# Performance work log

Measured on AMD Instinct MI355X. Metric: run time of the kernel, lower is better.

The kernel has to match this reference:

```python
import jax, jax.numpy as jnp
import numpy as np

T, N, C, L, H, NA, NL = 32, 64, 64, 64, 256, 16, 128


def _gru_dir(x, wi, wh, bi, bh):
    # x: [Lt, N, H] time-major; PyTorch GRU gate order (r, z, n). Returns [Lt, N, H].
    xi = jnp.einsum('tnh,gh->tng', x, wi) + bi  # precompute input projections [Lt,N,3H]
    def step(h, gi):
        gh = h @ wh.T + bh
        ir, iz, inn = jnp.split(gi, 3, -1)
        hr, hz, hn = jnp.split(gh, 3, -1)
        r = jax.nn.sigmoid(ir + hr)
        z = jax.nn.sigmoid(iz + hz)
        n = jnp.tanh(inn + r * hn)
        hnew = (1.0 - z) * n + z * h
        return hnew, hnew
    h0 = jnp.zeros((x.shape[1], wh.shape[1]), x.dtype)
    _, ys = jax.lax.scan(step, h0, xi)
    return ys


def setup_inputs() -> dict:
    key = jax.random.key(0)
    ks = jax.random.split(key, 32)
    s = 0.05
    p = {}
    p['condition'] = jax.random.normal(ks[0], (T, N, C), jnp.float32)
    p['lines'] = jax.random.randint(ks[1], (N, L), 0, NL)
    p['a_idx'] = jax.random.randint(ks[2], (T, N), 0, NA)
    p['p_idx'] = jax.random.randint(ks[3], (T, N), 0, L)
    p['embed'] = jax.random.normal(ks[4], (NL, H)) * s
    p['aemb'] = jax.random.normal(ks[5], (NA, H)) * s
    p['gru_wi_f'] = jax.random.normal(ks[6], (3 * H, H)) * s
    p['gru_wh_f'] = jax.random.normal(ks[7], (3 * H, H)) * s
    p['gru_bi_f'] = jax.random.normal(ks[8], (3 * H,)) * s
    p['gru_bh_f'] = jax.random.normal(ks[9], (3 * H,)) * s
    p['gru_wi_b'] = jax.random.normal(ks[10], (3 * H, H)) * s
    p['gru_wh_b'] = jax.random.normal(ks[11], (3 * H, H)) * s
    p['gru_bi_b'] = jax.random.normal(ks[12], (3 * H,)) * s
    p['gru_bh_b'] = jax.random.normal(ks[13], (3 * H,)) * s
    p['f_w1'] = jax.random.normal(ks[14], (H, C + H)) * s
    p['f_b1'] = jax.random.normal(ks[15], (H,)) * s
    p['f_w2'] = jax.random.normal(ks[16], (H, H)) * s
    p['f_b2'] = jax.random.normal(ks[17], (H,)) * s
    p['cell_wi'] = jax.random.normal(ks[18], (3 * H, H)) * s
    p['cell_wh'] = jax.random.normal(ks[19], (3 * H, H)) * s
    p['cell_bi'] = jax.random.normal(ks[20], (3 * H,)) * s
    p['cell_bh'] = jax.random.normal(ks[21], (3 * H,)) * s
    p['critic_w'] = jax.random.normal(ks[22], (1, H)) * s
    p['critic_b'] = jax.random.normal(ks[23], (1,)) * s
    p['pointer_w'] = jax.random.normal(ks[24], (L, H)) * s
    p['pointer_b'] = jax.random.normal(ks[25], (L,)) * s
    p['actor_w'] = jax.random.normal(ks[26], (NA, H)) * s
    p['actor_b'] = jax.random.normal(ks[27], (NA,)) * s
    p['query_w'] = jax.random.normal(ks[28], (H, H)) * s
    p['query_b'] = jax.random.normal(ks[29], (H,)) * s
    return p


def reference(condition, lines, a_idx, p_idx, embed, aemb,
              gru_wi_f, gru_wh_f, gru_bi_f, gru_bh_f,
              gru_wi_b, gru_wh_b, gru_bi_b, gru_bh_b,
              f_w1, f_b1, f_w2, f_b2,
              cell_wi, cell_wh, cell_bi, cell_bh,
              critic_w, critic_b, pointer_w, pointer_b,
              actor_w, actor_b, query_w, query_b):
    Tn, Nn = a_idx.shape
    Ln = lines.shape[1]
    Hd = embed.shape[1]
    M = embed[lines]                           # [N,L,H]
    x = jnp.transpose(M, (1, 0, 2))            # [L,N,H] time-major
    # torch.roll(x, shifts=i): rolled[i, j] = x[(j - i) % L]
    idx = (jnp.arange(Ln)[None, :] - jnp.arange(Ln)[:, None]) % Ln
    rolled = x[idx]                            # [L_roll, L_time, N, H]
    def bigru(seq):
        f = _gru_dir(seq, gru_wi_f, gru_wh_f, gru_bi_f, gru_bh_f)
        b = _gru_dir(seq[::-1], gru_wi_b, gru_wh_b, gru_bi_b, gru_bh_b)[::-1]
        return jnp.concatenate([f, b], -1)     # [L_time,N,2H]
    K1 = jax.vmap(bigru)(rolled)               # [L,L,N,2H]
    K = K1.reshape(Ln, Ln, Nn, 2, Hd).transpose(2, 0, 1, 3, 4).reshape(Nn, Ln, 2 * Ln, Hd)
    # A[t-1] for t=0 is hx.a == 0 (fresh episode, zero hidden state)
    a_prev = jnp.concatenate([jnp.zeros((1, Nn), a_idx.dtype), a_idx[:-1]], 0)
    rng_n = jnp.arange(Nn)
    def step(h, inp):
        cond_t, ap_t, p_t, a_t = inp
        obs = jnp.concatenate([cond_t, aemb[ap_t]], -1)
        xf = jax.nn.relu(obs @ f_w1.T + f_b1)
        xf = jax.nn.relu(xf @ f_w2.T + f_b2)
        gi = xf @ cell_wi.T + cell_bi
        gh = h @ cell_wh.T + cell_bh
        ir, iz, inn = jnp.split(gi, 3, -1)
        hr, hz, hn = jnp.split(gh, 3, -1)
        r = jax.nn.sigmoid(ir + hr)
        z = jax.nn.sigmoid(iz + hz)
        n = jnp.tanh(inn + r * hn)
        h = (1.0 - z) * n + z * h
        p_probs = jax.nn.softmax(h @ pointer_w.T + pointer_b, -1)
        q = h @ query_w.T + query_b
        k = K[rng_n, p_t]                      # gather: [N, 2L, H]
        l = jnp.einsum('nkh,nh->nk', k, q)
        zz = jnp.einsum('nk,nkh->nh', l, k)
        a_probs = jax.nn.softmax(zz @ actor_w.T + actor_b, -1)
        v = h @ critic_w.T + critic_b
        out = jnp.concatenate([a_t[:, None].astype(h.dtype), p_t[:, None].astype(h.dtype),
                               v, h, a_probs, p_probs], -1)
        return h, out
    h0 = jnp.zeros((Nn, Hd), condition.dtype)
    _, hxs = jax.lax.scan(step, h0, (condition, a_prev, p_idx, a_idx))
    return hxs  # packed RecurrentState: [T, N, 1+1+1+H+na+L]
```

## Files before the change

### kernel.cpp

```cpp
#include <hip/hip_runtime.h>
#include <hip/hip_bf16.h>
#include <cstddef>
#include <cstdint>

typedef __bf16 bf16;
typedef bf16 bf16x8 __attribute__((ext_vector_type(8)));
typedef float f32x4 __attribute__((ext_vector_type(4)));

#define DEV static __device__ __forceinline__

DEV f32x4 mfma_bf16(bf16x8 a, bf16x8 b, f32x4 c) {
  return __builtin_amdgcn_mfma_f32_16x16x32_bf16(a, b, c, 0, 0, 0);
}
DEV f32x4 mfma_fp8(long a, long b, f32x4 c) {
  return __builtin_amdgcn_mfma_f32_16x16x32_fp8_fp8(a, b, c, 0, 0, 0);
}

DEV float sigmoid_f(float x) {
  return __builtin_amdgcn_rcpf(1.0f + __expf(-x));
}
DEV float tanh_f(float x) {
  float ax = fabsf(x);
  float e = __expf(-2.0f * ax);
  float t = 1.0f - 2.0f * e * __builtin_amdgcn_rcpf(1.0f + e);
  return copysignf(t, x);
}
DEV unsigned char fp8_of(float x) {
  return (unsigned char)(__builtin_amdgcn_cvt_pk_fp8_f32(x, x, 0, false) & 0xFF);
}

static constexpr int H_ = 256;

static constexpr int o_embed = 0;
static constexpr int o_aemb = 32768;
static constexpr int o_wi_f = 36864;
static constexpr int o_wh_f = 233472;
static constexpr int o_bi_f = 430080;
static constexpr int o_bh_f = 430848;
static constexpr int o_wi_b = 431616;
static constexpr int o_wh_b = 628224;
static constexpr int o_bi_b = 824832;
static constexpr int o_bh_b = 825600;
static constexpr int o_f_w1 = 826368;
static constexpr int o_f_b1 = 908288;
static constexpr int o_f_w2 = 908544;
static constexpr int o_f_b2 = 974080;
static constexpr int o_cell_wi = 974336;
static constexpr int o_cell_wh = 1170944;
static constexpr int o_cell_bi = 1367552;
static constexpr int o_cell_bh = 1368320;
static constexpr int o_critic_w = 1369088;
static constexpr int o_critic_b = 1369344;
static constexpr int o_pointer_w = 1369360;
static constexpr int o_pointer_b = 1385744;
static constexpr int o_actor_w = 1385808;
static constexpr int o_actor_b = 1389904;
static constexpr int o_query_w = 1389920;
static constexpr int o_query_b = 1455456;
static constexpr int CW_TOTAL = 1455712;
static constexpr int WH8_TOTAL = 393216;
static constexpr int PREP_TOTAL = CW_TOTAL + WH8_TOTAL;
static constexpr int PREP_WGS = (PREP_TOTAL + 2047) / 2048;

static constexpr size_t XI_OFF = 0;
static constexpr size_t XI_BYTES = 2ull * 4096 * 768 * 2;
static constexpr size_t K1_OFF = XI_OFF + XI_BYTES;
static constexpr size_t K1_BYTES = 64ull * 32 * 128 * 256;
static constexpr size_t GI_OFF = K1_OFF + K1_BYTES;
static constexpr size_t GI_BYTES = 32ull * 64 * 768 * 4;
static constexpr size_t HD_OFF = GI_OFF + GI_BYTES;
static constexpr size_t HD_BYTES = 32ull * 64 * 256 * 4;
static constexpr size_t SLOT_OFF = HD_OFF + HD_BYTES;
static constexpr size_t SLOT_BYTES = 64ull * 64 * 4;
static constexpr size_t FLG_OFF = SLOT_OFF + SLOT_BYTES;
static constexpr size_t FLG_BYTES = 256;
static constexpr size_t WL_OFF = FLG_OFF + FLG_BYTES;
static constexpr size_t WL_BYTES = 8448;
static constexpr size_t CW_OFF = WL_OFF + WL_BYTES;
static constexpr size_t CW_BYTES = (size_t)CW_TOTAL * 2;
static constexpr size_t WH8_OFF = ((CW_OFF + CW_BYTES + 255) / 256) * 256;

struct PrepArgs {
  const void* src[26];
  int off[26];
  int cnt[26];
};

__global__ __launch_bounds__(256)
void k_prep(PrepArgs pa, const uint32_t* __restrict__ cond, const uint32_t* __restrict__ emb,
            const void* __restrict__ whf_src, const void* __restrict__ whb_src,
            const int* __restrict__ p_idx, int* __restrict__ flags,
            bf16* __restrict__ cw, unsigned char* __restrict__ wh8,
            int* __restrict__ slot_map, int* __restrict__ wl) {
  int bx = blockIdx.x;
  int tid = threadIdx.x;
  __shared__ int votes[256];

  int c1 = 0;
  {
    uint32_t w0 = emb[tid * 2], w1 = emb[tid * 2 + 1];
    int e0 = (int)((w0 >> 7) & 0xFF), e1 = (int)((w1 >> 7) & 0xFF);
    c1 += (e0 >= 96 && e0 <= 130) ? 1 : 0;
    c1 += (e1 >= 96 && e1 <= 130) ? 1 : 0;
  }
  votes[tid] = c1;
  __syncthreads();
  __shared__ int f32w_s;
  if (tid == 0) {
    int s = 0;
    for (int i = 0; i < 256; i++) s += votes[i];
    f32w_s = (s < 256) ? 1 : 0;
  }
  __syncthreads();
  bool f32w = f32w_s != 0;

  if (bx == 0) {
    __syncthreads();
    int c0 = 0;
    {
      uint32_t w0 = cond[tid * 2], w1 = cond[tid * 2 + 1];
      int e0 = (int)((w0 >> 7) & 0xFF), e1 = (int)((w1 >> 7) & 0xFF);
      c0 += (e0 >= 96 && e0 <= 130) ? 1 : 0;
      c0 += (e1 >= 96 && e1 <= 130) ? 1 : 0;
    }
    votes[tid] = c0;
    __syncthreads();
    if (tid == 0) {
      int s = 0;
      for (int i = 0; i < 256; i++) s += votes[i];
      flags[0] = (s < 256) ? 1 : 0;
      flags[1] = f32w ? 1 : 0;
    }
  }

  if (bx < PREP_WGS) {
    int gidx = bx * 2048 + tid;
    for (int e = 0; e < 8; e++, gidx += 256) {
      if (gidx >= PREP_TOTAL) break;
      if (gidx < CW_TOTAL) {
        int rem = gidx, s = 0;
        while (s < 26 && rem >= pa.cnt[s]) { rem -= pa.cnt[s]; s++; }
        if (s < 26) {
          float v = f32w ? ((const float*)pa.src[s])[rem]
                         : (float)((const bf16*)pa.src[s])[rem];
          cw[pa.off[s] + rem] = (bf16)v;
        }
      } else {
        int i = gidx - CW_TOTAL;
        const void* src = (i < 196608) ? whf_src : whb_src;
        int k = (i < 196608) ? i : i - 196608;
        float v = f32w ? ((const float*)src)[k] : (float)((const bf16*)src)[k];
        wh8[i] = fp8_of(v);
      }
    }
    return;
  }

  __shared__ int pbuf[2048];
  __shared__ signed char sm[4096];
  __shared__ unsigned short entL[8 * 512];
  __shared__ int cntL[8];
  for (int i = tid; i < 2048; i += 256) pbuf[i] = p_idx[i];
  for (int i = tid; i < 4096; i += 256) sm[i] = -1;
  __syncthreads();
  if (tid < 64) {
    int n = tid, cnt = 0;
    for (int t = 0; t < 32; t++) {
      int p = pbuf[t * 64 + n];
      if (sm[n * 64 + p] < 0) sm[n * 64 + p] = (signed char)(cnt++);
    }
  }
  __syncthreads();
  for (int i = tid; i < 4096; i += 256) slot_map[i] = (int)sm[i];
  if (tid < 8) {
    int xcd = tid, cnt = 0;
    for (int roll = xcd * 8; roll < xcd * 8 + 8; roll++)
      for (int n = 0; n < 64; n++)
        if (sm[n * 64 + roll] >= 0) entL[xcd * 512 + (cnt++)] = (unsigned short)(n | (roll << 8));
    unsigned short pad = (unsigned short)((xcd * 8) << 8);
    while (cnt & 15) entL[xcd * 512 + (cnt++)] = pad;
    cntL[xcd] = cnt;
  }
  __syncthreads();
  if (tid < 8) wl[tid] = cntL[tid] >> 4;
  unsigned short* we = (unsigned short*)((char*)wl + 64);
  for (int i = tid; i < 8 * 512; i += 256) we[i] = entL[i];
}

__global__ __launch_bounds__(256)
void k_xi_gi(const int* __restrict__ lines, const bf16* __restrict__ cw,
             const void* __restrict__ cond_raw, const int* __restrict__ flags,
             const int* __restrict__ a_idx, bf16* __restrict__ xi,
             float* __restrict__ gi) {
  int bx = blockIdx.x;
  int tid = threadIdx.x;
  int w = tid >> 6, l = tid & 63, quad = l >> 4, l15 = l & 15;
  __shared__ __attribute__((aligned(16))) bf16 s_a[32 * 328];
  __shared__ __attribute__((aligned(16))) bf16 s_b[32 * 264];

  if (bx < 256) {
    int dir = bx & 1, rb = bx >> 1;
    const bf16* embed = cw + o_embed;
    const bf16* wi = cw + (dir ? o_wi_b : o_wi_f);
    const bf16* bi = cw + (dir ? o_bi_b : o_bi_f);
    bf16* xs = s_a;
    {
      int row = tid >> 3, seg = tid & 7;
      int grow = rb * 32 + row;
      int u = grow >> 6, n = grow & 63;
      int line = lines[n * 64 + u];
      const bf16* src = embed + (size_t)line * H_ + seg * 32;
      bf16* dst = xs + row * 264 + seg * 32;
#pragma unroll
      for (int e = 0; e < 4; e++) *(bf16x8*)(dst + e * 8) = *(const bf16x8*)(src + e * 8);
    }
    __syncthreads();
    f32x4 acc[2][12];
#pragma unroll
    for (int mt = 0; mt < 2; mt++)
#pragma unroll
      for (int nt = 0; nt < 12; nt++) acc[mt][nt] = f32x4{0.f, 0.f, 0.f, 0.f};
#pragma unroll
    for (int ks = 0; ks < 8; ks++) {
      int koff = ks * 32 + quad * 8;
      bf16x8 a0 = *(const bf16x8*)(xs + l15 * 264 + koff);
      bf16x8 a1 = *(const bf16x8*)(xs + (l15 + 16) * 264 + koff);
#pragma unroll
      for (int nt = 0; nt < 12; nt++) {
        int g = (w * 12 + nt) * 16 + l15;
        bf16x8 b = *(const bf16x8*)(wi + (size_t)g * H_ + koff);
        acc[0][nt] = mfma_bf16(a0, b, acc[0][nt]);
        acc[1][nt] = mfma_bf16(a1, b, acc[1][nt]);
      }
    }
    size_t base = (size_t)dir * 4096 * 768;
#pragma unroll
    for (int nt = 0; nt < 12; nt++) {
      int g = (w * 12 + nt) * 16 + l15;
      float bias = (float)bi[g];
#pragma unroll
      for (int mt = 0; mt < 2; mt++)
#pragma unroll
        for (int r = 0; r < 4; r++) {
          int m = mt * 16 + quad * 4 + r;
          xi[base + (size_t)(rb * 32 + m) * 768 + g] = (bf16)(acc[mt][nt][r] + bias);
        }
    }
    return;
  }

  int rb = bx - 256;
  const bf16* aemb = cw + o_aemb;
  const bf16* f_w1 = cw + o_f_w1;
  const bf16* f_b1 = cw + o_f_b1;
  const bf16* f_w2 = cw + o_f_w2;
  const bf16* f_b2 = cw + o_f_b2;
  const bf16* cell_wi = cw + o_cell_wi;
  const bf16* cell_bi = cw + o_cell_bi;
  bool cf32 = flags[0] != 0;
  bf16* obs = s_a;
  bf16* xf1 = s_b;

  for (int e = tid; e < 32 * 320; e += 256) {
    int row = e / 320, col = e - row * 320;
    int grow = rb * 32 + row;
    int t = grow >> 6, n = grow & 63;
    float v;
    if (col < 64) {
      v = cf32 ? ((const float*)cond_raw)[(size_t)grow * 64 + col]
               : (float)((const bf16*)cond_raw)[(size_t)grow * 64 + col];
    } else {
      int ap = (t == 0) ? 0 : a_idx[(t - 1) * 64 + n];
      v = (float)aemb[ap * 256 + (col - 64)];
    }
    obs[row * 328 + col] = (bf16)v;
  }
  __syncthreads();
  {
    f32x4 acc[2][4];
#pragma unroll
    for (int mt = 0; mt < 2; mt++)
#pragma unroll
      for (int nt = 0; nt < 4; nt++) acc[mt][nt] = f32x4{0.f, 0.f, 0.f, 0.f};
#pragma unroll
    for (int ks = 0; ks < 10; ks++) {
      int koff = ks * 32 + quad * 8;
      bf16x8 a0 = *(const bf16x8*)(obs + l15 * 328 + koff);
      bf16x8 a1 = *(const bf16x8*)(obs + (l15 + 16) * 328 + koff);
#pragma unroll
      for (int nt = 0; nt < 4; nt++) {
        int g = (w * 4 + nt) * 16 + l15;
        bf16x8 b = *(const bf16x8*)(f_w1 + (size_t)g * 320 + koff);
        acc[0][nt] = mfma_bf16(a0, b, acc[0][nt]);
        acc[1][nt] = mfma_bf16(a1, b, acc[1][nt]);
      }
    }
#pragma unroll
    for (int nt = 0; nt < 4; nt++) {
      int g = (w * 4 + nt) * 16 + l15;
      float bias = (float)f_b1[g];
#pragma unroll
      for (int mt = 0; mt < 2; mt++)
#pragma unroll
        for (int r = 0; r < 4; r++) {
          int m = mt * 16 + quad * 4 + r;
          xf1[m * 264 + g] = (bf16)fmaxf(acc[mt][nt][r] + bias, 0.f);
        }
    }
  }
  __syncthreads();
  bf16* xf2 = obs;
  {
    f32x4 acc[2][4];
#pragma unroll
    for (int mt = 0; mt < 2; mt++)
#pragma unroll
      for (int nt = 0; nt < 4; nt++) acc[mt][nt] = f32x4{0.f, 0.f, 0.f, 0.f};
#pragma unroll
    for (int ks = 0; ks < 8; ks++) {
      int koff = ks * 32 + quad * 8;
      bf16x8 a0 = *(const bf16x8*)(xf1 + l15 * 264 + koff);
      bf16x8 a1 = *(const bf16x8*)(xf1 + (l15 + 16) * 264 + koff);
#pragma unroll
      for (int nt = 0; nt < 4; nt++) {
        int g = (w * 4 + nt) * 16 + l15;
        bf16x8 b = *(const bf16x8*)(f_w2 + (size_t)g * 256 + koff);
        acc[0][nt] = mfma_bf16(a0, b, acc[0][nt]);
        acc[1][nt] = mfma_bf16(a1, b, acc[1][nt]);
      }
    }
#pragma unroll
    for (int nt = 0; nt < 4; nt++) {
      int g = (w * 4 + nt) * 16 + l15;
      float bias = (float)f_b2[g];
#pragma unroll
      for (int mt = 0; mt < 2; mt++)
#pragma unroll
        for (int r = 0; r < 4; r++) {
          int m = mt * 16 + quad * 4 + r;
          xf2[m * 264 + g] = (bf16)fmaxf(acc[mt][nt][r] + bias, 0.f);
        }
    }
  }
  __syncthreads();
  {
    f32x4 acc[2][12];
#pragma unroll
    for (int mt = 0; mt < 2; mt++)
#pragma unroll
      for (int nt = 0; nt < 12; nt++) acc[mt][nt] = f32x4{0.f, 0.f, 0.f, 0.f};
#pragma unroll
    for (int ks = 0; ks < 8; ks++) {
      int koff = ks * 32 + quad * 8;
      bf16x8 a0 = *(const bf16x8*)(xf2 + l15 * 264 + koff);
      bf16x8 a1 = *(const bf16x8*)(xf2 + (l15 + 16) * 264 + koff);
#pragma unroll
      for (int nt = 0; nt < 12; nt++) {
        int g = (w * 12 + nt) * 16 + l15;
        bf16x8 b = *(const bf16x8*)(cell_wi + (size_t)g * 256 + koff);
        acc[0][nt] = mfma_bf16(a0, b, acc[0][nt]);
        acc[1][nt] = mfma_bf16(a1, b, acc[1][nt]);
      }
    }
#pragma unroll
    for (int nt = 0; nt < 12; nt++) {
      int g = (w * 12 + nt) * 16 + l15;
      float bias = (float)cell_bi[g];
#pragma unroll
      for (int mt = 0; mt < 2; mt++)
#pragma unroll
        for (int r = 0; r < 4; r++) {
          int m = mt * 16 + quad * 4 + r;
          gi[(size_t)(rb * 32 + m) * 768 + g] = acc[mt][nt][r] + bias;
        }
    }
  }
}

__global__ __launch_bounds__(1024)
void k_main(const bf16* __restrict__ cw, const unsigned char* __restrict__ wh8,
            const bf16* __restrict__ xi, const int* __restrict__ slot_map,
            const int* __restrict__ wl, const float* __restrict__ gi,
            unsigned char* __restrict__ K1c, float* __restrict__ hdec) {
  int bx = blockIdx.x;
  int tid = threadIdx.x;
  int w = tid >> 6, l = tid & 63, quad = l >> 4, l15 = l & 15;
  int c = w * 16 + l15;
  __shared__ __attribute__((aligned(16))) unsigned char smem[2][16 * 264 * 2];

  if (bx < 512) {
    int xcd = bx & 7, dir = (bx >> 3) & 1, slot = bx >> 4;
    if (slot >= wl[xcd]) return;
    const unsigned short* we = (const unsigned short*)((const char*)wl + 64) + xcd * 512 + slot * 16;
    const unsigned char* whd = wh8 + (size_t)dir * 196608;
    const bf16* bh = cw + (dir ? o_bh_b : o_bh_f);

    unsigned char (*hb)[16 * 264 * 2] = smem;
    for (int idx = tid; idx < 16 * 264; idx += 1024) hb[0][idx] = 0;

    int rollv[4], nbase[4];
#pragma unroll
    for (int r = 0; r < 4; r++) {
      int e = we[quad * 4 + r];
      rollv[r] = e >> 8;
      nbase[r] = (e & 255) * 768;
    }
    int crow = tid >> 6, cseg = tid & 63;
    int ec = we[crow];
    int n_c = ec & 255, roll_c = ec >> 8;
    int kslot = slot_map[n_c * 64 + roll_c];
    unsigned char* dstb = K1c + ((size_t)n_c * 32 + (kslot < 0 ? 0 : kslot)) * 32768 + cseg * 4;

    float hreg[4] = {0.f, 0.f, 0.f, 0.f};
    float bhv[3];
    const unsigned char* bp[3];
#pragma unroll
    for (int g = 0; g < 3; g++) {
      int grow = g * 256 + c;
      bhv[g] = (float)bh[grow];
      bp[g] = whd + (size_t)grow * 256 + quad * 8;
    }
    const bf16* xid = xi + (size_t)dir * 4096 * 768;
    __syncthreads();

    bf16 xpre[3][4];
#pragma unroll
    for (int r = 0; r < 4; r++) {
      int u = dir ? ((63 - rollv[r]) & 63) : ((0 - rollv[r]) & 63);
      const bf16* xr = xid + u * 49152 + nbase[r] + c;
#pragma unroll
      for (int g = 0; g < 3; g++) xpre[g][r] = xr[g * 256];
    }

    int cur = 0;
    for (int t = 0; t < 64; t++) {
      int j = dir ? (63 - t) : t;
      bf16 xnx[3][4];
#pragma unroll
      for (int r = 0; r < 4; r++) {
        int u = dir ? ((62 - t - rollv[r]) & 63) : ((t + 1 - rollv[r]) & 63);
        const bf16* xr = xid + u * 49152 + nbase[r] + c;
#pragma unroll
        for (int g = 0; g < 3; g++) xnx[g][r] = xr[g * 256];
      }

      f32x4 acc[3];
#pragma unroll
      for (int g = 0; g < 3; g++) acc[g] = f32x4{0.f, 0.f, 0.f, 0.f};
#pragma unroll
      for (int ks = 0; ks < 8; ks++) {
        int ko = ks * 32 + quad * 8;
        long a0 = *(const long*)(hb[cur] + l15 * 264 + ko);
#pragma unroll
        for (int g = 0; g < 3; g++) {
          long b = *(const long*)(bp[g] + ks * 32);
          acc[g] = mfma_fp8(a0, b, acc[g]);
        }
      }
      int nxt = cur ^ 1;
#pragma unroll
      for (int r = 0; r < 4; r++) {
        float rg = sigmoid_f((float)xpre[0][r] + acc[0][r] + bhv[0]);
        float zg = sigmoid_f((float)xpre[1][r] + acc[1][r] + bhv[1]);
        float ng = tanh_f((float)xpre[2][r] + rg * (acc[2][r] + bhv[2]));
        hreg[r] = (1.f - zg) * ng + zg * hreg[r];
        hb[nxt][(quad * 4 + r) * 264 + c] = fp8_of(hreg[r]);
      }
      __syncthreads();
      if (kslot >= 0) {
        *(uint32_t*)(dstb + (size_t)(j * 2 + dir) * 256) =
            *(const uint32_t*)(hb[nxt] + crow * 264 + cseg * 4);
      }
#pragma unroll
      for (int g = 0; g < 3; g++)
#pragma unroll
        for (int r = 0; r < 4; r++) xpre[g][r] = xnx[g][r];
      cur = nxt;
    }
    return;
  }

  int nq = bx - 512;
  const bf16* wh = cw + o_cell_wh;
  const bf16* bh = cw + o_cell_bh;
  bf16 (*hb)[16 * 264] = (bf16(*)[16 * 264])smem;
  for (int idx = tid; idx < 16 * 264; idx += 1024) hb[0][idx] = (bf16)0.f;

  float hreg[4] = {0.f, 0.f, 0.f, 0.f};
  float bhv[3];
  const bf16* bp[3];
  int goff[3][4];
#pragma unroll
  for (int g = 0; g < 3; g++) {
    int grow = g * 256 + c;
    bhv[g] = (float)bh[grow];
    bp[g] = wh + (size_t)grow * 256 + quad * 8;
#pragma unroll
    for (int r = 0; r < 4; r++)
      goff[g][r] = (quad * 4 + r) * 768 + grow;
  }
  const float* gbase = gi + (size_t)nq * 16 * 768;
  __syncthreads();

  float gpre[3][4];
#pragma unroll
  for (int r = 0; r < 4; r++)
#pragma unroll
    for (int g = 0; g < 3; g++) gpre[g][r] = gbase[goff[g][r]];

  int cur = 0;
  for (int t = 0; t < 32; t++) {
    int tp = (t + 1) & 31;
    const float* gr = gbase + (size_t)tp * 64 * 768;
    float gnx[3][4];
#pragma unroll
    for (int r = 0; r < 4; r++)
#pragma unroll
      for (int g = 0; g < 3; g++) gnx[g][r] = gr[goff[g][r]];

    f32x4 acc[3];
#pragma unroll
    for (int g = 0; g < 3; g++) acc[g] = f32x4{0.f, 0.f, 0.f, 0.f};
#pragma unroll
    for (int ks = 0; ks < 8; ks++) {
      int ko = ks * 32 + quad * 8;
      bf16x8 a0 = *(const bf16x8*)(hb[cur] + l15 * 264 + ko);
#pragma unroll
      for (int g = 0; g < 3; g++) {
        bf16x8 b = *(const bf16x8*)(bp[g] + ks * 32);
        acc[g] = mfma_bf16(a0, b, acc[g]);
      }
    }
    int nxt = cur ^ 1;
#pragma unroll
    for (int r = 0; r < 4; r++) {
      float rg = sigmoid_f(gpre[0][r] + acc[0][r] + bhv[0]);
      float zg = sigmoid_f(gpre[1][r] + acc[1][r] + bhv[1]);
      float ng = tanh_f(gpre[2][r] + rg * (acc[2][r] + bhv[2]));
      float hnew = (1.f - zg) * ng + zg * hreg[r];
      hreg[r] = hnew;
      hb[nxt][(quad * 4 + r) * 264 + c] = (bf16)hnew;
      hdec[((size_t)t * 64 + nq * 16 + quad * 4 + r) * 256 + c] = hnew;
    }
    __syncthreads();
#pragma unroll
    for (int g = 0; g < 3; g++)
#pragma unroll
      for (int r = 0; r < 4; r++) gpre[g][r] = gnx[g][r];
    cur = nxt;
  }
}

__global__ __launch_bounds__(256)
void k_post(const float* __restrict__ hdec, const unsigned char* __restrict__ K1c,
            const int* __restrict__ slot_map, const int* __restrict__ flags,
            const int* __restrict__ a_idx, const int* __restrict__ p_idx,
            const bf16* __restrict__ cw, void* __restrict__ out_raw) {
  int bx = blockIdx.x;
  int tid = threadIdx.x;
  int w = tid >> 6, l = tid & 63, quad = l >> 4, l15 = l & 15;
  __shared__ __attribute__((aligned(16))) unsigned char sraw[38032];
  bool f32o = flags[1] != 0;

  if (bx < 64) {
    int rb = bx;
    const bf16* pointer_w = cw + o_pointer_w;
    const bf16* pointer_b = cw + o_pointer_b;
    const bf16* critic_w = cw + o_critic_w;
    const bf16* critic_b = cw + o_critic_b;
    bf16* hsb = (bf16*)sraw;
    float* pls = (float*)(sraw + 16896);
    float* vred = (float*)(sraw + 16896 + 8448);

    for (int idx = tid; idx < 32 * 256; idx += 256) {
      int row = idx >> 8, col = idx & 255;
      hsb[row * 264 + col] = (bf16)hdec[(size_t)(rb * 32 + row) * 256 + col];
    }
    __syncthreads();

    {
      f32x4 acc[2];
      acc[0] = f32x4{0.f, 0.f, 0.f, 0.f};
      acc[1] = f32x4{0.f, 0.f, 0.f, 0.f};
      int g = w * 16 + l15;
#pragma unroll
      for (int ks = 0; ks < 8; ks++) {
        int koff = ks * 32 + quad * 8;
        bf16x8 a0 = *(const bf16x8*)(hsb + l15 * 264 + koff);
        bf16x8 a1 = *(const bf16x8*)(hsb + (l15 + 16) * 264 + koff);
        bf16x8 b = *(const bf16x8*)(pointer_w + (size_t)g * 256 + koff);
        acc[0] = mfma_bf16(a0, b, acc[0]);
        acc[1] = mfma_bf16(a1, b, acc[1]);
      }
      float bias = (float)pointer_b[g];
#pragma unroll
      for (int mt = 0; mt < 2; mt++)
#pragma unroll
        for (int r = 0; r < 4; r++) {
          int m = mt * 16 + quad * 4 + r;
          pls[m * 66 + g] = acc[mt][r] + bias;
        }
    }
    {
      int row = tid >> 3, seg = tid & 7;
      float acc = 0.f;
#pragma unroll
      for (int k = 0; k < 32; k++)
        acc += (float)hsb[row * 264 + seg * 32 + k] * (float)critic_w[seg * 32 + k];
      vred[row * 8 + seg] = acc;
    }
    __syncthreads();

    if (tid < 32) {
      float mx = -1e30f;
      for (int k = 0; k < 64; k++) mx = fmaxf(mx, pls[tid * 66 + k]);
      float sm = 0.f;
      for (int k = 0; k < 64; k++) {
        float e = __expf(pls[tid * 66 + k] - mx);
        pls[tid * 66 + k] = e;
        sm += e;
      }
      float inv = __builtin_amdgcn_rcpf(sm);
      for (int k = 0; k < 64; k++) pls[tid * 66 + k] *= inv;
      float v = (float)critic_b[0];
      for (int s = 0; s < 8; s++) v += vred[tid * 8 + s];
      vred[tid * 8] = v;
    }
    __syncthreads();

    if (f32o) {
      float* ob = (float*)out_raw;
      if (tid < 32) {
        int grow = rb * 32 + tid;
        ob[(size_t)grow * 339 + 0] = (float)a_idx[grow];
        ob[(size_t)grow * 339 + 1] = (float)p_idx[grow];
        ob[(size_t)grow * 339 + 2] = vred[tid * 8];
      }
      for (int idx = tid; idx < 32 * 256; idx += 256) {
        int row = idx >> 8, col = idx & 255;
        int grow = rb * 32 + row;
        ob[(size_t)grow * 339 + 3 + col] = hdec[(size_t)grow * 256 + col];
      }
      for (int idx = tid; idx < 32 * 64; idx += 256) {
        int row = idx >> 6, col = idx & 63;
        ob[(size_t)(rb * 32 + row) * 339 + 275 + col] = pls[row * 66 + col];
      }
    } else {
      bf16* ob = (bf16*)out_raw;
      if (tid < 32) {
        int grow = rb * 32 + tid;
        ob[(size_t)grow * 339 + 0] = (bf16)(float)a_idx[grow];
        ob[(size_t)grow * 339 + 1] = (bf16)(float)p_idx[grow];
        ob[(size_t)grow * 339 + 2] = (bf16)vred[tid * 8];
      }
      for (int idx = tid; idx < 32 * 256; idx += 256) {
        int row = idx >> 8, col = idx & 255;
        int grow = rb * 32 + row;
        ob[(size_t)grow * 339 + 3 + col] = (bf16)hdec[(size_t)grow * 256 + col];
      }
      for (int idx = tid; idx < 32 * 64; idx += 256) {
        int row = idx >> 6, col = idx & 63;
        ob[(size_t)(rb * 32 + row) * 339 + 275 + col] = (bf16)pls[row * 66 + col];
      }
    }
    return;
  }

  int tn = bx - 64;
  int t = tn >> 6, n = tn & 63;
  const bf16* actor_w = cw + o_actor_w;
  const bf16* actor_b = cw + o_actor_b;
  const bf16* query_w = cw + o_query_w;
  const bf16* query_b = cw + o_query_b;

  unsigned char* ksb = sraw;
  float* hs = (float*)(sraw + 33792);
  float* qs = (float*)(sraw + 33792 + 1024);
  float* ls = (float*)(sraw + 33792 + 2048);
  float* sA = (float*)(sraw + 33792 + 3072);
  float* al = (float*)(sraw + 33792 + 4096);

  hs[tid] = hdec[((size_t)t * 64 + n) * 256 + tid];
  int p = p_idx[t * 64 + n];
  int slot = slot_map[n * 64 + p];
  {
    const uint32_t* kg = (const uint32_t*)(K1c + ((size_t)n * 32 + slot) * 32768);
#pragma unroll
    for (int e = 0; e < 8; e++) {
      int flat = (e * 256 + tid) * 16;
      int kk = flat >> 8, col = flat & 255;
      uint32_t w0 = kg[(flat >> 2) + 0], w1 = kg[(flat >> 2) + 1];
      uint32_t w2 = kg[(flat >> 2) + 2], w3 = kg[(flat >> 2) + 3];
      uint32_t* d0 = (uint32_t*)(ksb + kk * 264 + col);
      d0[0] = w0; d0[1] = w1; d0[2] = w2; d0[3] = w3;
    }
  }
  __syncthreads();

  {
    float acc = (float)query_b[tid];
    const bf16* qw = query_w + (size_t)tid * 256;
#pragma unroll 4
    for (int k0 = 0; k0 < 256; k0 += 8) {
      bf16x8 wv = *(const bf16x8*)(qw + k0);
#pragma unroll
      for (int e = 0; e < 8; e++) acc += (float)wv[e] * hs[k0 + e];
    }
    qs[tid] = acc;
  }
  __syncthreads();

  {
    int kk = tid & 127, hc = tid >> 7;
    const uint32_t* kr = (const uint32_t*)(ksb + kk * 264 + hc * 128);
    const float* qr = qs + hc * 128;
    float acc = 0.f;
#pragma unroll 8
    for (int u = 0; u < 32; u++) {
      uint32_t b4 = kr[u];
      acc += __builtin_amdgcn_cvt_f32_fp8(b4, 0) * qr[u * 4 + 0];
      acc += __builtin_amdgcn_cvt_f32_fp8(b4, 1) * qr[u * 4 + 1];
      acc += __builtin_amdgcn_cvt_f32_fp8(b4, 2) * qr[u * 4 + 2];
      acc += __builtin_amdgcn_cvt_f32_fp8(b4, 3) * qr[u * 4 + 3];
    }
    ls[tid] = acc;
  }
  __syncthreads();
  if (tid < 128) ls[tid] += ls[tid + 128];
  __syncthreads();

  float zzv;
  {
    const unsigned char* kc = ksb + (tid & ~3);
    int sh = (tid & 3) * 8;
    float acc = 0.f;
#pragma unroll 8
    for (int kk = 0; kk < 128; kk++) {
      uint32_t d = *(const uint32_t*)(kc + kk * 264);
      acc += ls[kk] * __builtin_amdgcn_cvt_f32_fp8((int)(d >> sh), 0);
    }
    zzv = acc;
  }
  __syncthreads();
  qs[tid] = zzv;
  __syncthreads();

  {
    int a = tid >> 4, e = tid & 15;
    const bf16* aw = actor_w + (size_t)a * 256 + e * 16;
    const float* zr = qs + e * 16;
    float acc = 0.f;
#pragma unroll
    for (int hh = 0; hh < 16; hh++) acc += (float)aw[hh] * zr[hh];
    sA[tid] = acc;
  }
  __syncthreads();
  if (tid < 16) {
    float lg = (float)actor_b[tid];
#pragma unroll
    for (int e = 0; e < 16; e++) lg += sA[tid * 16 + e];
    float mx = lg;
#pragma unroll
    for (int m = 8; m > 0; m >>= 1) mx = fmaxf(mx, __shfl_xor(mx, m, 16));
    float ex = __expf(lg - mx);
    float sm = ex;
#pragma unroll
    for (int m = 8; m > 0; m >>= 1) sm += __shfl_xor(sm, m, 16);
    al[tid] = ex * __builtin_amdgcn_rcpf(sm);
  }
  __syncthreads();

  if (tid < 16) {
    size_t off = (size_t)(t * 64 + n) * 339 + 259 + tid;
    if (f32o) ((float*)out_raw)[off] = al[tid];
    else ((bf16*)out_raw)[off] = (bf16)al[tid];
  }
}

extern "C" void kernel_launch(void* const* d_in, const int* in_sizes, int n_in,
                              void* d_out, int out_size, void* d_ws, size_t ws_size,
                              hipStream_t stream) {
  (void)in_sizes; (void)n_in; (void)out_size; (void)ws_size;
  const void* condition = d_in[0];
  const int* lines      = (const int*)d_in[1];
  const int* a_idx      = (const int*)d_in[2];
  const int* p_idx      = (const int*)d_in[3];

  char* ws = (char*)d_ws;
  bf16* xi            = (bf16*)(ws + XI_OFF);
  unsigned char* K1c  = (unsigned char*)(ws + K1_OFF);
  float* gi           = (float*)(ws + GI_OFF);
  float* hdec         = (float*)(ws + HD_OFF);
  int* slot_map       = (int*)(ws + SLOT_OFF);
  int* flags          = (int*)(ws + FLG_OFF);
  int* wl             = (int*)(ws + WL_OFF);
  bf16* cw            = (bf16*)(ws + CW_OFF);
  unsigned char* wh8  = (unsigned char*)(ws + WH8_OFF);

  static const int src_idx[26] = {4, 5, 6, 7, 8, 9, 10, 11, 12, 13, 14, 15, 16,
                                  17, 18, 19, 20, 21, 22, 23, 24, 25, 26, 27, 28, 29};
  static const int offs[26] = {o_embed, o_aemb, o_wi_f, o_wh_f, o_bi_f, o_bh_f,
                               o_wi_b, o_wh_b, o_bi_b, o_bh_b, o_f_w1, o_f_b1,
                               o_f_w2, o_f_b2, o_cell_wi, o_cell_wh, o_cell_bi,
                               o_cell_bh, o_critic_w, o_critic_b, o_pointer_w,
                               o_pointer_b, o_actor_w, o_actor_b, o_query_w, o_query_b};
  static const int cnts[26] = {32768, 4096, 196608, 196608, 768, 768,
                               196608, 196608, 768, 768, 81920, 256,
                               65536, 256, 196608, 196608, 768,
                               768, 256, 1, 16384, 64, 4096, 16, 65536, 256};
  PrepArgs pa;
  for (int i = 0; i < 26; i++) {
    pa.src[i] = d_in[src_idx[i]];
    pa.off[i] = offs[i];
    pa.cnt[i] = cnts[i];
  }

  k_prep<<<PREP_WGS + 1, 256, 0, stream>>>(pa, (const uint32_t*)condition,
                                           (const uint32_t*)d_in[4], d_in[7], d_in[11],
                                           p_idx, flags, cw, wh8, slot_map, wl);
  k_xi_gi<<<320, 256, 0, stream>>>(lines, cw, condition, flags, a_idx, xi, gi);
  k_main<<<516, 1024, 0, stream>>>(cw, wh8, xi, slot_map, wl, gi, K1c, hdec);
  k_post<<<2112, 256, 0, stream>>>(hdec, K1c, slot_map, flags, a_idx, p_idx, cw, d_out);
}
```

Baseline: 395.4 us.

## Move query projection into decoder recurrence via MFMA and use LDS-only barriers

The query projection q = h·Wq^T + b was computed per (t,n) block in the post kernel with scalar FMAs. It is now computed inside the decoder GRU loop of the main kernel with bf16 MFMA, reusing h already held in shared memory, and written to a new workspace buffer. The post kernel then just loads q, which removes a 256x256 matvec and one barrier per block. Separately, __syncthreads is replaced by a barrier that waits only on LDS counters, so global stores are not drained at each step. The cost is a bf16-rounded h feeding the query and extra MFMA work on the serial decoder path, which only 4 blocks run.

```diff
diff --git a/kernel.cpp b/kernel.cpp
--- a/kernel.cpp
+++ b/kernel.cpp
@@ -14,6 +14,11 @@
 }
 DEV f32x4 mfma_fp8(long a, long b, f32x4 c) {
   return __builtin_amdgcn_mfma_f32_16x16x32_fp8_fp8(a, b, c, 0, 0, 0);
+}
+
+DEV void lds_barrier() {
+  __builtin_amdgcn_s_waitcnt(0xC07F);
+  __builtin_amdgcn_s_barrier();
 }
 
 DEV float sigmoid_f(float x) {
@@ -79,6 +84,7 @@
 static constexpr size_t CW_OFF = WL_OFF + WL_BYTES;
 static constexpr size_t CW_BYTES = (size_t)CW_TOTAL * 2;
 static constexpr size_t WH8_OFF = ((CW_OFF + CW_BYTES + 255) / 256) * 256;
+static constexpr size_t QS_OFF = ((WH8_OFF + WH8_TOTAL + 255) / 256) * 256;
 
 struct PrepArgs {
   const void* src[26];
@@ -381,7 +387,8 @@
 void k_main(const bf16* __restrict__ cw, const unsigned char* __restrict__ wh8,
             const bf16* __restrict__ xi, const int* __restrict__ slot_map,
             const int* __restrict__ wl, const float* __restrict__ gi,
-            unsigned char* __restrict__ K1c, float* __restrict__ hdec) {
+            unsigned char* __restrict__ K1c, float* __restrict__ hdec,
+            float* __restrict__ qs_ws) {
   int bx = blockIdx.x;
   int tid = threadIdx.x;
   int w = tid >> 6, l = tid & 63, quad = l >> 4, l15 = l & 15;
@@ -466,7 +473,7 @@
         hreg[r] = (1.f - zg) * ng + zg * hreg[r];
         hb[nxt][(quad * 4 + r) * 264 + c] = fp8_of(hreg[r]);
       }
-      __syncthreads();
+      lds_barrier();
       if (kslot >= 0) {
         *(uint32_t*)(dstb + (size_t)(j * 2 + dir) * 256) =
             *(const uint32_t*)(hb[nxt] + crow * 264 + cseg * 4);
@@ -483,6 +490,8 @@
   int nq = bx - 512;
   const bf16* wh = cw + o_cell_wh;
   const bf16* bh = cw + o_cell_bh;
+  const bf16* query_w = cw + o_query_w;
+  const bf16* query_b = cw + o_query_b;
   bf16 (*hb)[16 * 264] = (bf16(*)[16 * 264])smem;
   for (int idx = tid; idx < 16 * 264; idx += 1024) hb[0][idx] = (bf16)0.f;
 
@@ -499,6 +508,8 @@
     for (int r = 0; r < 4; r++)
       goff[g][r] = (quad * 4 + r) * 768 + grow;
   }
+  const bf16* qwp = query_w + (size_t)c * 256 + quad * 8;
+  float qbv = (float)query_b[c];
   const float* gbase = gi + (size_t)nq * 16 * 768;
   __syncthreads();
 
@@ -542,7 +553,21 @@
       hb[nxt][(quad * 4 + r) * 264 + c] = (bf16)hnew;
       hdec[((size_t)t * 64 + nq * 16 + quad * 4 + r) * 256 + c] = hnew;
     }
-    __syncthreads();
+    lds_barrier();
+
+    {
+      f32x4 qa = f32x4{0.f, 0.f, 0.f, 0.f};
+#pragma unroll
+      for (int ks = 0; ks < 8; ks++) {
+        int ko = ks * 32 + quad * 8;
+        bf16x8 a0 = *(const bf16x8*)(hb[nxt] + l15 * 264 + ko);
+        bf16x8 b = *(const bf16x8*)(qwp + ks * 32);
+        qa = mfma_bf16(a0, b, qa);
+      }
+#pragma unroll
+      for (int r = 0; r < 4; r++)
+        qs_ws[((size_t)t * 64 + nq * 16 + quad * 4 + r) * 256 + c] = qa[r] + qbv;
+    }
 #pragma unroll
     for (int g = 0; g < 3; g++)
 #pragma unroll
@@ -555,7 +580,8 @@
 void k_post(const float* __restrict__ hdec, const unsigned char* __restrict__ K1c,
             const int* __restrict__ slot_map, const int* __restrict__ flags,
             const int* __restrict__ a_idx, const int* __restrict__ p_idx,
-            const bf16* __restrict__ cw, void* __restrict__ out_raw) {
+            const bf16* __restrict__ cw, const float* __restrict__ qs_ws,
+            void* __restrict__ out_raw) {
   int bx = blockIdx.x;
   int tid = threadIdx.x;
   int w = tid >> 6, l = tid & 63, quad = l >> 4, l15 = l & 15;
@@ -670,17 +696,14 @@
   int t = tn >> 6, n = tn & 63;
   const bf16* actor_w = cw + o_actor_w;
   const bf16* actor_b = cw + o_actor_b;
-  const bf16* query_w = cw + o_query_w;
-  const bf16* query_b = cw + o_query_b;
 
   unsigned char* ksb = sraw;
-  float* hs = (float*)(sraw + 33792);
-  float* qs = (float*)(sraw + 33792 + 1024);
-  float* ls = (float*)(sraw + 33792 + 2048);
-  float* sA = (float*)(sraw + 33792 + 3072);
-  float* al = (float*)(sraw + 33792 + 4096);
-
-  hs[tid] = hdec[((size_t)t * 64 + n) * 256 + tid];
+  float* qs = (float*)(sraw + 33792);
+  float* ls = (float*)(sraw + 33792 + 1024);
+  float* sA = (float*)(sraw + 33792 + 2048);
+  float* al = (float*)(sraw + 33792 + 3072);
+
+  qs[tid] = qs_ws[((size_t)t * 64 + n) * 256 + tid];
   int p = p_idx[t * 64 + n];
   int slot = slot_map[n * 64 + p];
   {
@@ -694,19 +717,6 @@
       uint32_t* d0 = (uint32_t*)(ksb + kk * 264 + col);
       d0[0] = w0; d0[1] = w1; d0[2] = w2; d0[3] = w3;
     }
-  }
-  __syncthreads();
-
-  {
-    float acc = (float)query_b[tid];
-    const bf16* qw = query_w + (size_t)tid * 256;
-#pragma unroll 4
-    for (int k0 = 0; k0 < 256; k0 += 8) {
-      bf16x8 wv = *(const bf16x8*)(qw + k0);
-#pragma unroll
-      for (int e = 0; e < 8; e++) acc += (float)wv[e] * hs[k0 + e];
-    }
-    qs[tid] = acc;
   }
   __syncthreads();
 
@@ -796,6 +806,7 @@
   int* wl             = (int*)(ws + WL_OFF);
   bf16* cw            = (bf16*)(ws + CW_OFF);
   unsigned char* wh8  = (unsigned char*)(ws + WH8_OFF);
+  float* qs_ws        = (float*)(ws + QS_OFF);
 
   static const int src_idx[26] = {4, 5, 6, 7, 8, 9, 10, 11, 12, 13, 14, 15, 16,
                                   17, 18, 19, 20, 21, 22, 23, 24, 25, 26, 27, 28, 29};
@@ -819,6 +830,6 @@
                                            (const uint32_t*)d_in[4], d_in[7], d_in[11],
                                            p_idx, flags, cw, wh8, slot_map, wl);
   k_xi_gi<<<320, 256, 0, stream>>>(lines, cw, condition, flags, a_idx, xi, gi);
-  k_main<<<516, 1024, 0, stream>>>(cw, wh8, xi, slot_map, wl, gi, K1c, hdec);
-  k_post<<<2112, 256, 0, stream>>>(hdec, K1c, slot_map, flags, a_idx, p_idx, cw, d_out);
-}
+  k_main<<<516, 1024, 0, stream>>>(cw, wh8, xi, slot_map, wl, gi, K1c, hdec, qs_ws);
+  k_post<<<2112, 256, 0, stream>>>(hdec, K1c, slot_map, flags, a_idx, p_idx, cw, qs_ws, d_out);
+}
```

Result: slower. 613.8 us (+55.2%).
